# Performance work log

Measured on AMD Instinct MI355X. Metric: run time of the kernel, lower is better.

Reference implementation:

```python
import jax, jax.numpy as jnp
import numpy as np

BS, T, HS, WS = 2, 4, 32, 32
HW = HS * WS
D, NH, NL, NP = 256, 8, 4, 4
HD = D // NH
DFFN = 1024


def layer_norm(x, g, b, eps=1e-5):
    mu = jnp.mean(x, axis=-1, keepdims=True)
    var = jnp.mean((x - mu) ** 2, axis=-1, keepdims=True)
    return (x - mu) * jax.lax.rsqrt(var + eps) * g + b


def bilinear_gather(val, loc, Hl, Wl):
    # val: (bs, nh, Hl*Wl, hd); loc: (bs, Lq, nh, P, 2) in [0,1], last dim (x, y)
    # matches F.grid_sample(align_corners=False, padding_mode='zeros') on grid=2*loc-1
    x = loc[..., 0] * Wl - 0.5
    y = loc[..., 1] * Hl - 0.5
    x0 = jnp.floor(x)
    y0 = jnp.floor(y)
    lx = x - x0
    ly = y - y0
    bs, Lq, nh, P = x.shape
    out = jnp.zeros((bs, nh, Lq * P, val.shape[-1]), val.dtype)
    for dy in (0, 1):
        for dx in (0, 1):
            xi = x0 + dx
            yi = y0 + dy
            w = (lx if dx else 1.0 - lx) * (ly if dy else 1.0 - ly)
            valid = (xi >= 0) & (xi < Wl) & (yi >= 0) & (yi < Hl)
            w = jnp.where(valid, w, 0.0)
            xi_c = jnp.clip(xi, 0, Wl - 1).astype(jnp.int32)
            yi_c = jnp.clip(yi, 0, Hl - 1).astype(jnp.int32)
            idx = (yi_c * Wl + xi_c).transpose(0, 2, 1, 3).reshape(bs, nh, Lq * P)
            g = jnp.take_along_axis(val, idx[..., None], axis=2)
            wt = w.transpose(0, 2, 1, 3).reshape(bs, nh, Lq * P)
            out = out + wt[..., None] * g
    return out.reshape(bs, nh, Lq, P, val.shape[-1])


def setup_inputs() -> dict:
    key = jax.random.key(0)
    ks = jax.random.split(key, 12)
    s = 0.02
    return {
        "src": jax.random.normal(ks[0], (BS, T, HW, D), jnp.float32),
        "pos": jax.random.normal(ks[1], (BS, T, HW, D), jnp.float32),
        "reference_points": jax.random.uniform(ks[2], (BS, T * HW, NL, 2), jnp.float32),
        "value_proj_w": jax.random.normal(ks[3], (D, D), jnp.float32) * s,
        "value_proj_b": jnp.zeros((D,), jnp.float32),
        "sampling_offsets_w": jax.random.normal(ks[4], (D, NH * NL * NP * 2), jnp.float32) * s,
        "sampling_offsets_b": jax.random.normal(ks[5], (NH * NL * NP * 2,), jnp.float32) * s,
        "attn_weights_w": jax.random.normal(ks[6], (D, NH * NL * NP), jnp.float32) * s,
        "attn_weights_b": jnp.zeros((NH * NL * NP,), jnp.float32),
        "output_proj_w": jax.random.normal(ks[7], (D, D), jnp.float32) * s,
        "output_proj_b": jnp.zeros((D,), jnp.float32),
        "norm1_g": jnp.ones((D,), jnp.float32),
        "norm1_b": jnp.zeros((D,), jnp.float32),
        "linear1_w": jax.random.normal(ks[8], (D, DFFN), jnp.float32) * s,
        "linear1_b": jnp.zeros((DFFN,), jnp.float32),
        "linear2_w": jax.random.normal(ks[9], (DFFN, D), jnp.float32) * s,
        "linear2_b": jnp.zeros((D,), jnp.float32),
        "norm2_g": jnp.ones((D,), jnp.float32),
        "norm2_b": jnp.zeros((D,), jnp.float32),
        "spatial_shapes": np.array([[HS, WS]] * NL, np.int32),
        "level_start_index": np.arange(NL, dtype=np.int32) * HW,
    }


def reference(src, pos, reference_points, value_proj_w, value_proj_b,
              sampling_offsets_w, sampling_offsets_b, attn_weights_w, attn_weights_b,
              output_proj_w, output_proj_b, norm1_g, norm1_b,
              linear1_w, linear1_b, linear2_w, linear2_b, norm2_g, norm2_b,
              spatial_shapes, level_start_index):
    bs, t, hw, d = src.shape
    Lq = t * hw
    x = src.reshape(bs, Lq, d)
    q = x  # module never adds pos in forward (with_pos_embed unused)
    value = (x @ value_proj_w + value_proj_b).reshape(bs, Lq, NH, HD)
    offsets = (q @ sampling_offsets_w + sampling_offsets_b).reshape(bs, Lq, NH, NL, NP, 2)
    aw = jax.nn.softmax((q @ attn_weights_w + attn_weights_b).reshape(bs, Lq, NH, NL * NP), axis=-1)
    aw = aw.reshape(bs, Lq, NH, NL, NP)
    ss = np.asarray(spatial_shapes)
    lsi = np.asarray(level_start_index)
    offset_normalizer = jnp.asarray(ss[:, ::-1].copy(), src.dtype)  # (L, 2) = (W, H)
    sampling_locations = reference_points[:, :, None, :, None, :] + offsets / offset_normalizer[None, None, None, :, None, :]
    attn_out = jnp.zeros((bs, NH, Lq, HD), src.dtype)
    for l in range(NL):
        Hl, Wl = int(ss[l, 0]), int(ss[l, 1])
        start = int(lsi[l])
        v_l = value[:, start:start + Hl * Wl].transpose(0, 2, 1, 3)  # (bs, nh, HlWl, hd)
        samp = bilinear_gather(v_l, sampling_locations[:, :, :, l], Hl, Wl)  # (bs, nh, Lq, P, hd)
        w_l = aw[:, :, :, l].transpose(0, 2, 1, 3)  # (bs, nh, Lq, P)
        attn_out = attn_out + jnp.sum(samp * w_l[..., None], axis=3)
    attn_out = attn_out.transpose(0, 2, 1, 3).reshape(bs, Lq, d) @ output_proj_w + output_proj_b
    x = layer_norm(x + attn_out, norm1_g, norm1_b)
    ffn = jax.nn.relu(x @ linear1_w + linear1_b) @ linear2_w + linear2_b
    x = layer_norm(x + ffn, norm2_g, norm2_b)
    return x.reshape(bs, t, hw, d), sampling_locations
```

## Files before the change

### kernel.cpp

```cpp
#include <hip/hip_runtime.h>
#include <math.h>

#define ROWS   8192
#define LQ     4096
#define NHEAD  8
#define NLVL   4
#define NPTS   4
#define HDIM   32

typedef __attribute__((ext_vector_type(8))) short v8s;
typedef __attribute__((ext_vector_type(4))) float v4f;

__device__ __forceinline__ unsigned short f2bf(float x) {
    unsigned int u = __float_as_uint(x);
    u += 0x7fffu + ((u >> 16) & 1u);
    return (unsigned short)(u >> 16);
}
__device__ __forceinline__ float bf2f(unsigned short x) {
    return __uint_as_float(((unsigned int)x) << 16);
}

__device__ __forceinline__ void glds16(const void* g, void* l) {
    __builtin_amdgcn_global_load_lds(
        (const __attribute__((address_space(1))) unsigned int*)g,
        (__attribute__((address_space(3))) unsigned int*)l, 16, 0, 0);
}

__device__ __forceinline__ void trans_tile(const float* __restrict__ in,
                                           unsigned short* __restrict__ out,
                                           int K, int N, int ldout, int n_off,
                                           int bx, int by, int tid)
{
    __shared__ float t[32][33];
    int tx = tid & 31, ty = tid >> 5;
    int k0 = by << 5, n0 = bx << 5;
    #pragma unroll
    for (int i = 0; i < 4; i++)
        t[ty + i * 8][tx] = in[(size_t)(k0 + ty + i * 8) * N + n0 + tx];
    __syncthreads();
    #pragma unroll
    for (int i = 0; i < 4; i++)
        out[(size_t)(n_off + n0 + ty + i * 8) * ldout + k0 + tx] = f2bf(t[tx][ty + i * 8]);
}

__global__ __launch_bounds__(256) void prep_k(
    const float* __restrict__ src, unsigned short* __restrict__ src_bf,
    const float* __restrict__ vw, const float* __restrict__ ofw,
    const float* __restrict__ aww, const float* __restrict__ pw,
    const float* __restrict__ w1, const float* __restrict__ w2,
    unsigned short* __restrict__ Btcat, unsigned short* __restrict__ pwT,
    unsigned short* __restrict__ w1T, unsigned short* __restrict__ w2T,
    const float* __restrict__ vb, const float* __restrict__ ofb,
    const float* __restrict__ awb, float* __restrict__ biascat)
{
    int bid = blockIdx.x, tid = threadIdx.x;
    if (bid < 2048) {
        int i = bid * 256 + tid;
        float4 v = ((const float4*)src)[i];
        ushort4 o;
        o.x = f2bf(v.x); o.y = f2bf(v.y); o.z = f2bf(v.z); o.w = f2bf(v.w);
        ((ushort4*)src_bf)[i] = o;
    } else if (bid < 2112) {
        int t = bid - 2048; trans_tile(vw, Btcat, 256, 256, 256, 0, t & 7, t >> 3, tid);
    } else if (bid < 2176) {
        int t = bid - 2112; trans_tile(ofw, Btcat, 256, 256, 256, 256, t & 7, t >> 3, tid);
    } else if (bid < 2208) {
        int t = bid - 2176; trans_tile(aww, Btcat, 256, 128, 256, 512, t & 3, t >> 2, tid);
    } else if (bid < 2272) {
        int t = bid - 2208; trans_tile(pw, pwT, 256, 256, 256, 0, t & 7, t >> 3, tid);
    } else if (bid < 2528) {
        int t = bid - 2272; trans_tile(w1, w1T, 256, 1024, 256, 0, t & 31, t >> 5, tid);
    } else if (bid < 2784) {
        int t = bid - 2528; trans_tile(w2, w2T, 1024, 256, 1024, 0, t & 7, t >> 3, tid);
    } else {
        biascat[tid] = vb[tid];
        biascat[tid + 256] = ofb[tid];
        if (tid < 128) biascat[tid + 512] = awb[tid];
    }
}

template<bool PROJ, bool OUTBF, bool RELU, bool RES>
__global__ __launch_bounds__(256) void mfma_gemm_k(
    const unsigned short* __restrict__ A,
    const unsigned short* __restrict__ Bt,
    const float* __restrict__ bias,
    const float* __restrict__ res,
    void* __restrict__ Cout,
    unsigned short* __restrict__ vbf,
    const float* __restrict__ refp,
    float* __restrict__ oloc,
    int M, int N, int K)
{
    __shared__ __align__(16) unsigned short As[4096];
    __shared__ __align__(16) unsigned short Bs[2048];
    const int tid = threadIdx.x;
    const int row0 = blockIdx.y << 7, col0 = blockIdx.x << 6;
    const int wid = tid >> 6, lane = tid & 63;
    const int wm = wid & 1, wn = wid >> 1;
    const int lr = lane & 15, kq = lane >> 4;

    v4f acc[4][2];
    #pragma unroll
    for (int i = 0; i < 4; i++)
        #pragma unroll
        for (int j = 0; j < 2; j++) acc[i][j] = (v4f){0.f, 0.f, 0.f, 0.f};

    for (int k0 = 0; k0 < K; k0 += 32) {
        __syncthreads();
        #pragma unroll
        for (int i = 0; i < 2; i++) {
            int c = wid * 128 + i * 64 + lane;
            int row = c >> 2;
            int kk = ((c & 3) + (row >> 2)) & 3;
            glds16(A + (size_t)(row0 + row) * K + k0 + kk * 8,
                   &As[(wid * 128 + i * 64) * 8]);
        }
        {
            int c = wid * 64 + lane;
            int row = c >> 2;
            int kk = ((c & 3) + (row >> 2)) & 3;
            glds16(Bt + (size_t)(col0 + row) * K + k0 + kk * 8,
                   &Bs[wid * 512]);
        }
        __syncthreads();
        v8s bf[2];
        #pragma unroll
        for (int nt = 0; nt < 2; nt++) {
            int row = wn * 32 + nt * 16 + lr;
            int s = (kq - (row >> 2)) & 3;
            bf[nt] = *(const v8s*)(&Bs[(row * 4 + s) * 8]);
        }
        #pragma unroll
        for (int mt = 0; mt < 4; mt++) {
            int row = wm * 64 + mt * 16 + lr;
            int s = (kq - (row >> 2)) & 3;
            v8s af = *(const v8s*)(&As[(row * 4 + s) * 8]);
            #pragma unroll
            for (int nt = 0; nt < 2; nt++)
                acc[mt][nt] = __builtin_amdgcn_mfma_f32_16x16x32_bf16(af, bf[nt], acc[mt][nt], 0, 0, 0);
        }
    }

    const int rq = lane >> 4;
    #pragma unroll
    for (int mt = 0; mt < 4; mt++) {
        #pragma unroll
        for (int nt = 0; nt < 2; nt++) {
            int col = col0 + wn * 32 + nt * 16 + lr;
            float bv = bias[col];
            #pragma unroll
            for (int i = 0; i < 4; i++) {
                int row = row0 + wm * 64 + mt * 16 + rq * 4 + i;
                float v = acc[mt][nt][i] + bv;
                if (RELU) v = fmaxf(v, 0.f);
                if (RES)  v += res[(size_t)row * N + col];
                if (PROJ) {
                    if (col0 < 256) {
                        int b = row >> 12, rb = row & 4095;
                        int l = rb >> 10, pix = rb & 1023;
                        int h = col >> 5, d = col & 31;
                        size_t idx = ((size_t)(((b << 2) + l) * 8 + h) << 15) + (pix << 5) + d;
                        vbf[idx] = f2bf(v);
                    } else if (col0 < 512) {
                        int colm = col - 256;
                        int l = (colm >> 3) & 3, cc = colm & 1;
                        oloc[(size_t)row * 256 + colm] =
                            refp[(size_t)row * 8 + l * 2 + cc] + v * (1.f / 32.f);
                    } else {
                        ((float*)Cout)[(size_t)row * 128 + col - 512] = v;
                    }
                } else if (OUTBF) {
                    ((unsigned short*)Cout)[(size_t)row * N + col] = f2bf(v);
                } else {
                    ((float*)Cout)[(size_t)row * N + col] = v;
                }
            }
        }
    }
}

template<bool OUTBF, bool RELU, bool RES>
__global__ __launch_bounds__(256) void mfma_gemm64_k(
    const unsigned short* __restrict__ A,
    const unsigned short* __restrict__ Bt,
    const float* __restrict__ bias,
    const float* __restrict__ res,
    void* __restrict__ Cout,
    int M, int N, int K)
{
    __shared__ __align__(16) unsigned short As[2048];
    __shared__ __align__(16) unsigned short Bs[2048];
    const int tid = threadIdx.x;
    const int row0 = blockIdx.y << 6, col0 = blockIdx.x << 6;
    const int wid = tid >> 6, lane = tid & 63;
    const int lr = lane & 15, kq = lane >> 4;

    v4f acc[4];
    #pragma unroll
    for (int i = 0; i < 4; i++) acc[i] = (v4f){0.f, 0.f, 0.f, 0.f};

    for (int k0 = 0; k0 < K; k0 += 32) {
        __syncthreads();
        {
            int c = wid * 64 + lane;
            int row = c >> 2;
            int kk = ((c & 3) + (row >> 2)) & 3;
            glds16(A + (size_t)(row0 + row) * K + k0 + kk * 8, &As[wid * 512]);
            glds16(Bt + (size_t)(col0 + row) * K + k0 + kk * 8, &Bs[wid * 512]);
        }
        __syncthreads();
        int colr = wid * 16 + lr;
        int sb = (kq - (colr >> 2)) & 3;
        v8s bf = *(const v8s*)(&Bs[(colr * 4 + sb) * 8]);
        #pragma unroll
        for (int mt = 0; mt < 4; mt++) {
            int rowr = mt * 16 + lr;
            int sa = (kq - (rowr >> 2)) & 3;
            v8s af = *(const v8s*)(&As[(rowr * 4 + sa) * 8]);
            acc[mt] = __builtin_amdgcn_mfma_f32_16x16x32_bf16(af, bf, acc[mt], 0, 0, 0);
        }
    }

    const int rq = lane >> 4;
    const int col = col0 + wid * 16 + lr;
    float bv = bias[col];
    #pragma unroll
    for (int mt = 0; mt < 4; mt++) {
        #pragma unroll
        for (int i = 0; i < 4; i++) {
            int row = row0 + mt * 16 + rq * 4 + i;
            float v = acc[mt][i] + bv;
            if (RELU) v = fmaxf(v, 0.f);
            if (RES)  v += res[(size_t)row * N + col];
            if (OUTBF) ((unsigned short*)Cout)[(size_t)row * N + col] = f2bf(v);
            else       ((float*)Cout)[(size_t)row * N + col] = v;
        }
    }
}

template<bool WRITE_BF>
__global__ __launch_bounds__(256) void mfma_gemm_ln_k(
    const unsigned short* __restrict__ A,
    const unsigned short* __restrict__ Bt,
    const float* __restrict__ bias,
    const float* __restrict__ res,
    const float* __restrict__ g,
    const float* __restrict__ b,
    float* __restrict__ out,
    unsigned short* __restrict__ outbf,
    int M, int K)
{
    __shared__ __align__(16) unsigned short As[1024];
    __shared__ __align__(16) unsigned short Bs[8192];
    __shared__ float red[2][32][4];
    const int tid = threadIdx.x;
    const int row0 = blockIdx.x << 5;
    const int wid = tid >> 6, lane = tid & 63;
    const int lr = lane & 15, kq = lane >> 4;
    const int rq = kq;

    v4f acc[2][4];
    #pragma unroll
    for (int i = 0; i < 2; i++)
        #pragma unroll
        for (int j = 0; j < 4; j++) acc[i][j] = (v4f){0.f, 0.f, 0.f, 0.f};

    for (int k0 = 0; k0 < K; k0 += 32) {
        __syncthreads();
        if (wid < 2) {
            int c = wid * 64 + lane;
            int row = c >> 2;
            int kk = ((c & 3) + (row >> 2)) & 3;
            glds16(A + (size_t)(row0 + row) * K + k0 + kk * 8,
                   &As[(wid * 64) * 8]);
        }
        #pragma unroll
        for (int i = 0; i < 4; i++) {
            int c = (wid * 4 + i) * 64 + lane;
            int col = c >> 2;
            int kk = ((c & 3) + (col >> 2)) & 3;
            glds16(Bt + (size_t)col * K + k0 + kk * 8,
                   &Bs[((wid * 4 + i) * 64) * 8]);
        }
        __syncthreads();
        v8s bf[4];
        #pragma unroll
        for (int ct = 0; ct < 4; ct++) {
            int col = wid * 64 + ct * 16 + lr;
            int s = (kq - (col >> 2)) & 3;
            bf[ct] = *(const v8s*)(&Bs[(col * 4 + s) * 8]);
        }
        #pragma unroll
        for (int rt = 0; rt < 2; rt++) {
            int rowl = rt * 16 + lr;
            int s = (kq - (rowl >> 2)) & 3;
            v8s af = *(const v8s*)(&As[(rowl * 4 + s) * 8]);
            #pragma unroll
            for (int ct = 0; ct < 4; ct++)
                acc[rt][ct] = __builtin_amdgcn_mfma_f32_16x16x32_bf16(af, bf[ct], acc[rt][ct], 0, 0, 0);
        }
    }

    float t[2][4][4];
    float s1[2][4], s2[2][4];
    #pragma unroll
    for (int rt = 0; rt < 2; rt++)
        #pragma unroll
        for (int i = 0; i < 4; i++) { s1[rt][i] = 0.f; s2[rt][i] = 0.f; }
    #pragma unroll
    for (int rt = 0; rt < 2; rt++) {
        #pragma unroll
        for (int ct = 0; ct < 4; ct++) {
            int col = wid * 64 + ct * 16 + lr;
            float bv = bias[col];
            #pragma unroll
            for (int i = 0; i < 4; i++) {
                int row = row0 + rt * 16 + rq * 4 + i;
                float v = acc[rt][ct][i] + bv + res[(size_t)row * 256 + col];
                t[rt][ct][i] = v;
                s1[rt][i] += v;
                s2[rt][i] += v * v;
            }
        }
    }
    #pragma unroll
    for (int o = 1; o < 16; o <<= 1) {
        #pragma unroll
        for (int rt = 0; rt < 2; rt++)
            #pragma unroll
            for (int i = 0; i < 4; i++) {
                s1[rt][i] += __shfl_xor(s1[rt][i], o);
                s2[rt][i] += __shfl_xor(s2[rt][i], o);
            }
    }
    if (lr == 0) {
        #pragma unroll
        for (int rt = 0; rt < 2; rt++)
            #pragma unroll
            for (int i = 0; i < 4; i++) {
                int rl = rt * 16 + rq * 4 + i;
                red[0][rl][wid] = s1[rt][i];
                red[1][rl][wid] = s2[rt][i];
            }
    }
    __syncthreads();
    float mu[2][4], rstd[2][4];
    #pragma unroll
    for (int rt = 0; rt < 2; rt++) {
        #pragma unroll
        for (int i = 0; i < 4; i++) {
            int rl = rt * 16 + rq * 4 + i;
            float S1 = red[0][rl][0] + red[0][rl][1] + red[0][rl][2] + red[0][rl][3];
            float S2 = red[1][rl][0] + red[1][rl][1] + red[1][rl][2] + red[1][rl][3];
            float m = S1 * (1.f / 256.f);
            mu[rt][i] = m;
            rstd[rt][i] = rsqrtf(S2 * (1.f / 256.f) - m * m + 1e-5f);
        }
    }
    #pragma unroll
    for (int rt = 0; rt < 2; rt++) {
        #pragma unroll
        for (int ct = 0; ct < 4; ct++) {
            int col = wid * 64 + ct * 16 + lr;
            float gg = g[col], bb = b[col];
            #pragma unroll
            for (int i = 0; i < 4; i++) {
                int row = row0 + rt * 16 + rq * 4 + i;
                float o = (t[rt][ct][i] - mu[rt][i]) * rstd[rt][i] * gg + bb;
                out[(size_t)row * 256 + col] = o;
                if (WRITE_BF) outbf[(size_t)row * 256 + col] = f2bf(o);
            }
        }
    }
}

__global__ __launch_bounds__(256) void fused_gather_k(
    const float* __restrict__ po,
    const unsigned short* __restrict__ vbf,
    const float* __restrict__ loc,
    unsigned short* __restrict__ attn_bf)
{
    int tid = threadIdx.x;
    int u = tid >> 5, l = (tid >> 3) & 3, d4 = tid & 7;
    int h = blockIdx.x & 7;
    int r = (blockIdx.x >> 3) * 8 + u;
    int b = r >> 12;

    float locv[8];
    *(float4*)(locv)     = *(const float4*)(loc + (size_t)r * 256 + h * 32 + l * 8);
    *(float4*)(locv + 4) = *(const float4*)(loc + (size_t)r * 256 + h * 32 + l * 8 + 4);

    float w4[4];
    *(float4*)(w4) = *(const float4*)(po + (size_t)r * 128 + h * 16 + l * 4);
    float m = fmaxf(fmaxf(w4[0], w4[1]), fmaxf(w4[2], w4[3]));
    m = fmaxf(m, __shfl_xor(m, 8));
    m = fmaxf(m, __shfl_xor(m, 16));
    float s = 0.f;
    #pragma unroll
    for (int p = 0; p < 4; p++) { w4[p] = __expf(w4[p] - m); s += w4[p]; }
    s += __shfl_xor(s, 8);
    s += __shfl_xor(s, 16);
    float inv = 1.f / s;

    const unsigned short* vbase =
        vbf + (((size_t)(((b << 2) + l) * 8 + h)) << 15) + d4 * 4;
    ushort4 uv[16];
    float cw[16];
    #pragma unroll
    for (int p = 0; p < 4; p++) {
        float xf = locv[p * 2] * 32.f - 0.5f, yf = locv[p * 2 + 1] * 32.f - 0.5f;
        float x0f = floorf(xf), y0f = floorf(yf);
        float fx = xf - x0f, fy = yf - y0f;
        int x0 = (int)x0f, y0 = (int)y0f;
        float wgt = w4[p] * inv;
        #pragma unroll
        for (int dy = 0; dy < 2; dy++) {
            #pragma unroll
            for (int dx = 0; dx < 2; dx++) {
                int idx = p * 4 + dy * 2 + dx;
                int xi = x0 + dx, yi = y0 + dy;
                float wt = (dx ? fx : 1.f - fx) * (dy ? fy : 1.f - fy);
                bool valid = (xi >= 0) & (xi < 32) & (yi >= 0) & (yi < 32);
                int xc = min(max(xi, 0), 31), yc = min(max(yi, 0), 31);
                cw[idx] = valid ? (wgt * wt) : 0.f;
                uv[idx] = *(const ushort4*)(vbase + (size_t)((yc << 5) + xc) * 32);
            }
        }
    }
    float4 acc = {0.f, 0.f, 0.f, 0.f};
    #pragma unroll
    for (int idx = 0; idx < 16; idx++) {
        float c = cw[idx];
        acc.x += c * bf2f(uv[idx].x); acc.y += c * bf2f(uv[idx].y);
        acc.z += c * bf2f(uv[idx].z); acc.w += c * bf2f(uv[idx].w);
    }
    acc.x += __shfl_xor(acc.x, 8);  acc.y += __shfl_xor(acc.y, 8);
    acc.z += __shfl_xor(acc.z, 8);  acc.w += __shfl_xor(acc.w, 8);
    acc.x += __shfl_xor(acc.x, 16); acc.y += __shfl_xor(acc.y, 16);
    acc.z += __shfl_xor(acc.z, 16); acc.w += __shfl_xor(acc.w, 16);
    if (l == 0) {
        ushort4 o;
        o.x = f2bf(acc.x); o.y = f2bf(acc.y); o.z = f2bf(acc.z); o.w = f2bf(acc.w);
        *(ushort4*)(attn_bf + (size_t)r * 256 + h * 32 + d4 * 4) = o;
    }
}

template<bool WRITE_BF>
__global__ __launch_bounds__(256) void layernorm_k(
    float* __restrict__ x, const float* __restrict__ g, const float* __restrict__ b,
    unsigned short* __restrict__ xbf)
{
    int lane = threadIdx.x & 63;
    int wv = threadIdx.x >> 6;
    int row = blockIdx.x * 4 + wv;
    int c = lane << 2;
    float4 v = *(const float4*)(x + (size_t)row * 256 + c);
    float s = v.x + v.y + v.z + v.w;
    #pragma unroll
    for (int o = 1; o < 64; o <<= 1) s += __shfl_xor(s, o);
    float mu = s * (1.f / 256.f);
    float d0 = v.x - mu, d1 = v.y - mu, d2 = v.z - mu, d3 = v.w - mu;
    float vs = d0 * d0 + d1 * d1 + d2 * d2 + d3 * d3;
    #pragma unroll
    for (int o = 1; o < 64; o <<= 1) vs += __shfl_xor(vs, o);
    float rstd = rsqrtf(vs * (1.f / 256.f) + 1e-5f);
    float4 gg = *(const float4*)(g + c);
    float4 bb = *(const float4*)(b + c);
    float4 o4;
    o4.x = d0 * rstd * gg.x + bb.x;
    o4.y = d1 * rstd * gg.y + bb.y;
    o4.z = d2 * rstd * gg.z + bb.z;
    o4.w = d3 * rstd * gg.w + bb.w;
    *(float4*)(x + (size_t)row * 256 + c) = o4;
    if (WRITE_BF) {
        ushort4 ob;
        ob.x = f2bf(o4.x); ob.y = f2bf(o4.y); ob.z = f2bf(o4.z); ob.w = f2bf(o4.w);
        *(ushort4*)(xbf + (size_t)row * 256 + c) = ob;
    }
}

extern "C" void kernel_launch(void* const* d_in, const int* in_sizes, int n_in,
                              void* d_out, int out_size, void* d_ws, size_t ws_size,
                              hipStream_t stream)
{
    const float* src   = (const float*)d_in[0];
    const float* refp  = (const float*)d_in[2];
    const float* vw    = (const float*)d_in[3];
    const float* vb    = (const float*)d_in[4];
    const float* ofw   = (const float*)d_in[5];
    const float* ofb   = (const float*)d_in[6];
    const float* aww   = (const float*)d_in[7];
    const float* awb   = (const float*)d_in[8];
    const float* pw    = (const float*)d_in[9];
    const float* pb    = (const float*)d_in[10];
    const float* g1    = (const float*)d_in[11];
    const float* b1    = (const float*)d_in[12];
    const float* w1    = (const float*)d_in[13];
    const float* bi1   = (const float*)d_in[14];
    const float* w2    = (const float*)d_in[15];
    const float* bi2   = (const float*)d_in[16];
    const float* g2    = (const float*)d_in[17];
    const float* b2    = (const float*)d_in[18];

    float* ws = (float*)d_ws;
    float*          po        = ws;
    float*          x1        = ws + 1048576;
    unsigned short* value_bf  = (unsigned short*)(ws + 3145728);
    unsigned short* src_bf    = (unsigned short*)(ws + 4194304);
    unsigned short* x1_bf     = (unsigned short*)(ws + 5242880);
    unsigned short* attn_bf   = (unsigned short*)(ws + 6291456);
    unsigned short* hidden_bf = (unsigned short*)(ws + 7340032);
    unsigned short* Btcat     = (unsigned short*)(ws + 11534336);
    unsigned short* pwT       = (unsigned short*)(ws + 11616256);
    unsigned short* w1T       = (unsigned short*)(ws + 11649024);
    unsigned short* w2T       = (unsigned short*)(ws + 11780096);
    float*          biascat   = ws + 11911168;

    float* out_x   = (float*)d_out;
    float* out_loc = out_x + 2097152;

    dim3 blk(256);

    prep_k<<<2785, blk, 0, stream>>>(src, src_bf, vw, ofw, aww, pw, w1, w2,
                                     Btcat, pwT, w1T, w2T, vb, ofb, awb, biascat);

    mfma_gemm_k<true, false, false, false><<<dim3(10, 64), blk, 0, stream>>>(
        src_bf, Btcat, biascat, nullptr, po, value_bf, refp, out_loc, ROWS, 640, 256);

    fused_gather_k<<<8192, blk, 0, stream>>>(po, value_bf, out_loc, attn_bf);

    mfma_gemm_ln_k<true><<<256, blk, 0, stream>>>(
        attn_bf, pwT, pb, src, g1, b1, x1, x1_bf, ROWS, 256);

    mfma_gemm_k<false, true, true, false><<<dim3(16, 64), blk, 0, stream>>>(
        x1_bf, w1T, bi1, nullptr, hidden_bf, nullptr, nullptr, nullptr, ROWS, 1024, 256);

    mfma_gemm64_k<false, false, true><<<dim3(4, 128), blk, 0, stream>>>(
        hidden_bf, w2T, bi2, x1, out_x, ROWS, 256, 1024);
    layernorm_k<false><<<2048, blk, 0, stream>>>(out_x, g2, b2, nullptr);
}
```

Measured before the change: 188.6 us.

## Fuse src bf16 conversion into projection GEMM and widen gather loads

Removes the separate src fp32→bf16 conversion pass from the prep kernel. The first projection GEMM now loads fp32 A tiles into registers and converts them to bf16 before storing to LDS, replacing the async global-to-LDS path for that operand. Separately, the deformable gather kernel now has each thread load 8 bf16 channels (16 bytes) instead of 4 and processes 16 rows per block with half the blocks, which cuts lane count and shuffle work. The trade-off is double the A read bytes in the GEMM, register-staged loads that lose the direct-to-LDS path, and higher register pressure in the gather.

Result: faster. 182.4 us (-3.3%).

```diff
diff --git a/kernel.cpp b/kernel.cpp
--- a/kernel.cpp
+++ b/kernel.cpp
@@ -10,6 +10,7 @@
 
 typedef __attribute__((ext_vector_type(8))) short v8s;
 typedef __attribute__((ext_vector_type(4))) float v4f;
+typedef __attribute__((ext_vector_type(8))) unsigned short v8u;
 
 __device__ __forceinline__ unsigned short f2bf(float x) {
     unsigned int u = __float_as_uint(x);
@@ -44,7 +45,6 @@
 }
 
 __global__ __launch_bounds__(256) void prep_k(
-    const float* __restrict__ src, unsigned short* __restrict__ src_bf,
     const float* __restrict__ vw, const float* __restrict__ ofw,
     const float* __restrict__ aww, const float* __restrict__ pw,
     const float* __restrict__ w1, const float* __restrict__ w2,
@@ -54,24 +54,18 @@
     const float* __restrict__ awb, float* __restrict__ biascat)
 {
     int bid = blockIdx.x, tid = threadIdx.x;
-    if (bid < 2048) {
-        int i = bid * 256 + tid;
-        float4 v = ((const float4*)src)[i];
-        ushort4 o;
-        o.x = f2bf(v.x); o.y = f2bf(v.y); o.z = f2bf(v.z); o.w = f2bf(v.w);
-        ((ushort4*)src_bf)[i] = o;
-    } else if (bid < 2112) {
-        int t = bid - 2048; trans_tile(vw, Btcat, 256, 256, 256, 0, t & 7, t >> 3, tid);
-    } else if (bid < 2176) {
-        int t = bid - 2112; trans_tile(ofw, Btcat, 256, 256, 256, 256, t & 7, t >> 3, tid);
-    } else if (bid < 2208) {
-        int t = bid - 2176; trans_tile(aww, Btcat, 256, 128, 256, 512, t & 3, t >> 2, tid);
-    } else if (bid < 2272) {
-        int t = bid - 2208; trans_tile(pw, pwT, 256, 256, 256, 0, t & 7, t >> 3, tid);
-    } else if (bid < 2528) {
-        int t = bid - 2272; trans_tile(w1, w1T, 256, 1024, 256, 0, t & 31, t >> 5, tid);
-    } else if (bid < 2784) {
-        int t = bid - 2528; trans_tile(w2, w2T, 1024, 256, 1024, 0, t & 7, t >> 3, tid);
+    if (bid < 64) {
+        int t = bid; trans_tile(vw, Btcat, 256, 256, 256, 0, t & 7, t >> 3, tid);
+    } else if (bid < 128) {
+        int t = bid - 64; trans_tile(ofw, Btcat, 256, 256, 256, 256, t & 7, t >> 3, tid);
+    } else if (bid < 160) {
+        int t = bid - 128; trans_tile(aww, Btcat, 256, 128, 256, 512, t & 3, t >> 2, tid);
+    } else if (bid < 224) {
+        int t = bid - 160; trans_tile(pw, pwT, 256, 256, 256, 0, t & 7, t >> 3, tid);
+    } else if (bid < 480) {
+        int t = bid - 224; trans_tile(w1, w1T, 256, 1024, 256, 0, t & 31, t >> 5, tid);
+    } else if (bid < 736) {
+        int t = bid - 480; trans_tile(w2, w2T, 1024, 256, 1024, 0, t & 7, t >> 3, tid);
     } else {
         biascat[tid] = vb[tid];
         biascat[tid + 256] = ofb[tid];
@@ -79,9 +73,9 @@
     }
 }
 
-template<bool PROJ, bool OUTBF, bool RELU, bool RES>
+template<bool PROJ, bool AF32, bool OUTBF, bool RELU, bool RES>
 __global__ __launch_bounds__(256) void mfma_gemm_k(
-    const unsigned short* __restrict__ A,
+    const void* __restrict__ Araw,
     const unsigned short* __restrict__ Bt,
     const float* __restrict__ bias,
     const float* __restrict__ res,
@@ -106,14 +100,36 @@
         for (int j = 0; j < 2; j++) acc[i][j] = (v4f){0.f, 0.f, 0.f, 0.f};
 
     for (int k0 = 0; k0 < K; k0 += 32) {
+        float4 af0, af1, af2, af3;
+        if constexpr (AF32) {
+            const float* Af = (const float*)Araw;
+            int r1 = tid >> 2, kk1 = ((tid & 3) + (r1 >> 2)) & 3;
+            int c2 = tid + 256;
+            int r2 = c2 >> 2, kk2 = ((c2 & 3) + (r2 >> 2)) & 3;
+            const float* p1 = Af + (size_t)(row0 + r1) * K + k0 + kk1 * 8;
+            const float* p2 = Af + (size_t)(row0 + r2) * K + k0 + kk2 * 8;
+            af0 = *(const float4*)p1; af1 = *(const float4*)(p1 + 4);
+            af2 = *(const float4*)p2; af3 = *(const float4*)(p2 + 4);
+        }
         __syncthreads();
-        #pragma unroll
-        for (int i = 0; i < 2; i++) {
-            int c = wid * 128 + i * 64 + lane;
-            int row = c >> 2;
-            int kk = ((c & 3) + (row >> 2)) & 3;
-            glds16(A + (size_t)(row0 + row) * K + k0 + kk * 8,
-                   &As[(wid * 128 + i * 64) * 8]);
+        if constexpr (AF32) {
+            v8u u1, u2;
+            u1[0] = f2bf(af0.x); u1[1] = f2bf(af0.y); u1[2] = f2bf(af0.z); u1[3] = f2bf(af0.w);
+            u1[4] = f2bf(af1.x); u1[5] = f2bf(af1.y); u1[6] = f2bf(af1.z); u1[7] = f2bf(af1.w);
+            u2[0] = f2bf(af2.x); u2[1] = f2bf(af2.y); u2[2] = f2bf(af2.z); u2[3] = f2bf(af2.w);
+            u2[4] = f2bf(af3.x); u2[5] = f2bf(af3.y); u2[6] = f2bf(af3.z); u2[7] = f2bf(af3.w);
+            *(v8u*)(&As[tid * 8]) = u1;
+            *(v8u*)(&As[(tid + 256) * 8]) = u2;
+        } else {
+            const unsigned short* A = (const unsigned short*)Araw;
+            #pragma unroll
+            for (int i = 0; i < 2; i++) {
+                int c = wid * 128 + i * 64 + lane;
+                int row = c >> 2;
+                int kk = ((c & 3) + (row >> 2)) & 3;
+                glds16(A + (size_t)(row0 + row) * K + k0 + kk * 8,
+                       &As[(wid * 128 + i * 64) * 8]);
+            }
         }
         {
             int c = wid * 64 + lane;
@@ -381,9 +397,9 @@
     unsigned short* __restrict__ attn_bf)
 {
     int tid = threadIdx.x;
-    int u = tid >> 5, l = (tid >> 3) & 3, d4 = tid & 7;
+    int g = tid >> 4, l = (tid >> 2) & 3, d8 = tid & 3;
     int h = blockIdx.x & 7;
-    int r = (blockIdx.x >> 3) * 8 + u;
+    int r = (blockIdx.x >> 3) * 16 + g;
     int b = r >> 12;
 
     float locv[8];
@@ -393,55 +409,66 @@
     float w4[4];
     *(float4*)(w4) = *(const float4*)(po + (size_t)r * 128 + h * 16 + l * 4);
     float m = fmaxf(fmaxf(w4[0], w4[1]), fmaxf(w4[2], w4[3]));
+    m = fmaxf(m, __shfl_xor(m, 4));
     m = fmaxf(m, __shfl_xor(m, 8));
-    m = fmaxf(m, __shfl_xor(m, 16));
     float s = 0.f;
     #pragma unroll
     for (int p = 0; p < 4; p++) { w4[p] = __expf(w4[p] - m); s += w4[p]; }
+    s += __shfl_xor(s, 4);
     s += __shfl_xor(s, 8);
-    s += __shfl_xor(s, 16);
     float inv = 1.f / s;
 
     const unsigned short* vbase =
-        vbf + (((size_t)(((b << 2) + l) * 8 + h)) << 15) + d4 * 4;
-    ushort4 uv[16];
-    float cw[16];
-    #pragma unroll
-    for (int p = 0; p < 4; p++) {
-        float xf = locv[p * 2] * 32.f - 0.5f, yf = locv[p * 2 + 1] * 32.f - 0.5f;
-        float x0f = floorf(xf), y0f = floorf(yf);
-        float fx = xf - x0f, fy = yf - y0f;
-        int x0 = (int)x0f, y0 = (int)y0f;
-        float wgt = w4[p] * inv;
-        #pragma unroll
-        for (int dy = 0; dy < 2; dy++) {
-            #pragma unroll
-            for (int dx = 0; dx < 2; dx++) {
-                int idx = p * 4 + dy * 2 + dx;
-                int xi = x0 + dx, yi = y0 + dy;
-                float wt = (dx ? fx : 1.f - fx) * (dy ? fy : 1.f - fy);
-                bool valid = (xi >= 0) & (xi < 32) & (yi >= 0) & (yi < 32);
-                int xc = min(max(xi, 0), 31), yc = min(max(yi, 0), 31);
-                cw[idx] = valid ? (wgt * wt) : 0.f;
-                uv[idx] = *(const ushort4*)(vbase + (size_t)((yc << 5) + xc) * 32);
-            }
-        }
-    }
-    float4 acc = {0.f, 0.f, 0.f, 0.f};
-    #pragma unroll
-    for (int idx = 0; idx < 16; idx++) {
-        float c = cw[idx];
-        acc.x += c * bf2f(uv[idx].x); acc.y += c * bf2f(uv[idx].y);
-        acc.z += c * bf2f(uv[idx].z); acc.w += c * bf2f(uv[idx].w);
-    }
-    acc.x += __shfl_xor(acc.x, 8);  acc.y += __shfl_xor(acc.y, 8);
-    acc.z += __shfl_xor(acc.z, 8);  acc.w += __shfl_xor(acc.w, 8);
-    acc.x += __shfl_xor(acc.x, 16); acc.y += __shfl_xor(acc.y, 16);
-    acc.z += __shfl_xor(acc.z, 16); acc.w += __shfl_xor(acc.w, 16);
+        vbf + (((size_t)(((b << 2) + l) * 8 + h)) << 15) + d8 * 8;
+
+    float acc[8];
+    #pragma unroll
+    for (int k = 0; k < 8; k++) acc[k] = 0.f;
+
+    #pragma unroll
+    for (int pp = 0; pp < 2; pp++) {
+        v8u uv[8];
+        float cw[8];
+        #pragma unroll
+        for (int p2 = 0; p2 < 2; p2++) {
+            int p = pp * 2 + p2;
+            float xf = locv[p * 2] * 32.f - 0.5f, yf = locv[p * 2 + 1] * 32.f - 0.5f;
+            float x0f = floorf(xf), y0f = floorf(yf);
+            float fx = xf - x0f, fy = yf - y0f;
+            int x0 = (int)x0f, y0 = (int)y0f;
+            float wgt = w4[p] * inv;
+            #pragma unroll
+            for (int dy = 0; dy < 2; dy++) {
+                #pragma unroll
+                for (int dx = 0; dx < 2; dx++) {
+                    int idx = p2 * 4 + dy * 2 + dx;
+                    int xi = x0 + dx, yi = y0 + dy;
+                    float wt = (dx ? fx : 1.f - fx) * (dy ? fy : 1.f - fy);
+                    bool valid = (xi >= 0) & (xi < 32) & (yi >= 0) & (yi < 32);
+                    int xc = min(max(xi, 0), 31), yc = min(max(yi, 0), 31);
+                    cw[idx] = valid ? (wgt * wt) : 0.f;
+                    uv[idx] = *(const v8u*)(vbase + (size_t)((yc << 5) + xc) * 32);
+                }
+            }
+        }
+        #pragma unroll
+        for (int idx = 0; idx < 8; idx++) {
+            float c = cw[idx];
+            #pragma unroll
+            for (int k = 0; k < 8; k++)
+                acc[k] += c * bf2f(uv[idx][k]);
+        }
+    }
+    #pragma unroll
+    for (int k = 0; k < 8; k++) {
+        acc[k] += __shfl_xor(acc[k], 4);
+        acc[k] += __shfl_xor(acc[k], 8);
+    }
     if (l == 0) {
-        ushort4 o;
-        o.x = f2bf(acc.x); o.y = f2bf(acc.y); o.z = f2bf(acc.z); o.w = f2bf(acc.w);
-        *(ushort4*)(attn_bf + (size_t)r * 256 + h * 32 + d4 * 4) = o;
+        v8u o;
+        #pragma unroll
+        for (int k = 0; k < 8; k++) o[k] = f2bf(acc[k]);
+        *(v8u*)(attn_bf + (size_t)r * 256 + h * 32 + d8 * 8) = o;
     }
 }
 
@@ -506,7 +533,6 @@
     float*          po        = ws;
     float*          x1        = ws + 1048576;
     unsigned short* value_bf  = (unsigned short*)(ws + 3145728);
-    unsigned short* src_bf    = (unsigned short*)(ws + 4194304);
     unsigned short* x1_bf     = (unsigned short*)(ws + 5242880);
     unsigned short* attn_bf   = (unsigned short*)(ws + 6291456);
     unsigned short* hidden_bf = (unsigned short*)(ws + 7340032);
@@ -521,18 +547,18 @@
 
     dim3 blk(256);
 
-    prep_k<<<2785, blk, 0, stream>>>(src, src_bf, vw, ofw, aww, pw, w1, w2,
-                                     Btcat, pwT, w1T, w2T, vb, ofb, awb, biascat);
-
-    mfma_gemm_k<true, false, false, false><<<dim3(10, 64), blk, 0, stream>>>(
-        src_bf, Btcat, biascat, nullptr, po, value_bf, refp, out_loc, ROWS, 640, 256);
-
-    fused_gather_k<<<8192, blk, 0, stream>>>(po, value_bf, out_loc, attn_bf);
+    prep_k<<<737, blk, 0, stream>>>(vw, ofw, aww, pw, w1, w2,
+                                    Btcat, pwT, w1T, w2T, vb, ofb, awb, biascat);
+
+    mfma_gemm_k<true, true, false, false, false><<<dim3(10, 64), blk, 0, stream>>>(
+        src, Btcat, biascat, nullptr, po, value_bf, refp, out_loc, ROWS, 640, 256);
+
+    fused_gather_k<<<4096, blk, 0, stream>>>(po, value_bf, out_loc, attn_bf);
 
     mfma_gemm_ln_k<true><<<256, blk, 0, stream>>>(
         attn_bf, pwT, pb, src, g1, b1, x1, x1_bf, ROWS, 256);
 
-    mfma_gemm_k<false, true, true, false><<<dim3(16, 64), blk, 0, stream>>>(
+    mfma_gemm_k<false, false, true, true, false><<<dim3(16, 64), blk, 0, stream>>>(
         x1_bf, w1T, bi1, nullptr, hidden_bf, nullptr, nullptr, nullptr, ROWS, 1024, 256);
 
     mfma_gemm64_k<false, false, true><<<dim3(4, 128), blk, 0, stream>>>(
```
